# Optimization experiments

Measured on AMD Instinct MI355X. Metric: run time of the kernel, lower is better.

The kernel has to match this reference:

```python
import jax, jax.numpy as jnp
import numpy as np

T, B, NHID = 64, 32, 768
NB, BS = 6, 128          # num_blocks, block_size = nhid // num_blocks
TOPK = 4                 # active blocks per step
NTOK = 32000
ATT = 4 * BS             # input-attention value dim (att_out), per RIMs BlocksCore
DK = 64                  # input-attention key dim
NH2, DK2 = 4, 16         # communication attention heads / head dim


def setup_inputs() -> dict:
    key = jax.random.key(0)
    ks = jax.random.split(key, 16)
    s = 0.02
    return {
        "x": jax.random.normal(ks[0], (T, B, NHID), jnp.float32),
        "hx0": jax.random.normal(ks[1], (B, NHID), jnp.float32),
        "cx0": jax.random.normal(ks[2], (B, NHID), jnp.float32),
        # input attention (1 head): per-read-block query proj, per-write-slot key/value proj
        "Wq_in": jax.random.normal(ks[3], (NB, BS, DK), jnp.float32) * s,
        "Wk_in": jax.random.normal(ks[4], (2, NHID, DK), jnp.float32) * s,
        "Wv_in": jax.random.normal(ks[5], (2, NHID, ATT), jnp.float32) * s,
        # block-diagonal LSTM (blockify_params): per-block weights
        "Wih": jax.random.normal(ks[6], (NB, ATT, 4 * BS), jnp.float32) * s,
        "Whh": jax.random.normal(ks[7], (NB, BS, 4 * BS), jnp.float32) * s,
        "b_lstm": jnp.zeros((NB, 4 * BS), jnp.float32),
        # communication attention (4 heads, dk=dv=16), per-block projections + output proj
        "Wq_c": jax.random.normal(ks[8], (NB, BS, NH2 * DK2), jnp.float32) * s,
        "Wk_c": jax.random.normal(ks[9], (NB, BS, NH2 * DK2), jnp.float32) * s,
        "Wv_c": jax.random.normal(ks[10], (NB, BS, NH2 * DK2), jnp.float32) * s,
        "Wo_c": jax.random.normal(ks[11], (NB, NH2 * DK2, BS), jnp.float32) * s,
        # decoder
        "Wd": jax.random.normal(ks[12], (NTOK, NHID), jnp.float32) * 0.1,
        "bd": jnp.zeros((NTOK,), jnp.float32),
    }


def _step(hx, cx, xt, Wq_in, Wk_in, Wv_in, Wih, Whh, b_lstm, Wq_c, Wk_c, Wv_c, Wo_c):
    hb = hx.reshape(B, NB, BS)
    cb = cx.reshape(B, NB, BS)
    # --- input attention: each block reads from {null, input} slots ---
    kv_in = jnp.stack([jnp.zeros_like(xt), xt], axis=1)          # [B,2,NHID]
    q = jnp.einsum('bnd,ndk->bnk', hb, Wq_in)                    # [B,NB,DK]
    k = jnp.einsum('bmd,mdk->bmk', kv_in, Wk_in)                 # [B,2,DK]
    v = jnp.einsum('bmd,mdv->bmv', kv_in, Wv_in)                 # [B,2,ATT]
    iatt = jax.nn.softmax(
        jnp.einsum('bnk,bmk->bnm', q, k) / jnp.sqrt(jnp.float32(DK)), axis=-1)
    inp_use = jnp.einsum('bnm,bmv->bnv', iatt, v)                # [B,NB,ATT]
    # --- top-k block routing: drop NB-TOPK blocks attending most to null ---
    null_att = iatt[:, :, 0]                                     # [B,NB]
    _, drop_idx = jax.lax.top_k(null_att, NB - TOPK)
    mask = jnp.ones((B, NB), hx.dtype).at[
        jnp.arange(B)[:, None], drop_idx].set(0.0)               # [B,NB]
    # --- per-block (block-diagonal) LSTM ---
    gates = (jnp.einsum('bnv,nvg->bng', inp_use, Wih)
             + jnp.einsum('bnh,nhg->bng', hb, Whh) + b_lstm)     # [B,NB,4*BS]
    i, f, g, o = jnp.split(gates, 4, axis=-1)
    c_new = jax.nn.sigmoid(f) * cb + jax.nn.sigmoid(i) * jnp.tanh(g)
    h_new = jax.nn.sigmoid(o) * jnp.tanh(c_new)                  # [B,NB,BS]
    # --- communication attention among blocks (residual) ---
    q2 = jnp.einsum('bnd,ndk->bnk', h_new, Wq_c).reshape(B, NB, NH2, DK2)
    k2 = jnp.einsum('bnd,ndk->bnk', h_new, Wk_c).reshape(B, NB, NH2, DK2)
    v2 = jnp.einsum('bnd,ndk->bnk', h_new, Wv_c).reshape(B, NB, NH2, DK2)
    att = jax.nn.softmax(
        jnp.einsum('bihk,bjhk->bhij', q2, k2) / jnp.sqrt(jnp.float32(DK2)), axis=-1)
    comm = jnp.einsum('bhij,bjhv->bihv', att, v2).reshape(B, NB, NH2 * DK2)
    h_new = h_new + jnp.einsum('bnk,nkd->bnd', comm, Wo_c)
    # --- gated state update: inactive blocks keep old state ---
    m = mask[:, :, None]
    hx_next = (m * h_new + (1.0 - m) * hb).reshape(B, NHID)
    cx_next = (m * c_new + (1.0 - m) * cb).reshape(B, NHID)
    return hx_next, cx_next


def reference(x, hx0, cx0, Wq_in, Wk_in, Wv_in, Wih, Whh, b_lstm,
              Wq_c, Wk_c, Wv_c, Wo_c, Wd, bd):
    def scan_step(carry, xt):
        hx, cx = carry
        hx, cx = _step(hx, cx, xt, Wq_in, Wk_in, Wv_in, Wih, Whh, b_lstm,
                       Wq_c, Wk_c, Wv_c, Wo_c)
        return (hx, cx), hx
    (hx, cx), outs = jax.lax.scan(scan_step, (hx0, cx0), x)     # outs: [T,B,NHID]
    decoded = outs.reshape(T * B, NHID) @ Wd.T + bd              # [T*B,NTOK]
    return decoded, hx, cx
```

## Files before the change

### kernel.cpp

```cpp
#include <hip/hip_runtime.h>
#include <hip/hip_bf16.h>
#include <stdint.h>

#define TT 64
#define BB 32
#define NHIDC 768
#define NBK 6
#define BSZ 128
#define NTOKC 32000

using f32x4  = __attribute__((ext_vector_type(4))) float;
using f32x2  = __attribute__((ext_vector_type(2))) float;
using short8 = __attribute__((ext_vector_type(8))) short;
typedef unsigned long long u64;

#define OFF_XPUB  4096u
#define OFF_HTB   8065024u
#define OFF_K1    11210752u
#define OFF_V1    11735040u
#define OFF_U     15929344u
#define OFF_WDB   41095168u

__device__ __forceinline__ float sigf(float x){ return 1.f/(1.f + expf(-x)); }

__device__ __forceinline__ void stp(u64* p, float v, unsigned tag){
  union { float f; unsigned u; } cv; cv.f = v;
  const u64 pk = ((u64)tag << 32) | cv.u;
  __hip_atomic_store(p, pk, __ATOMIC_RELAXED, __HIP_MEMORY_SCOPE_AGENT);
}
__device__ __forceinline__ float ldp(const u64* p, unsigned tag){
  u64 v = __hip_atomic_load(p, __ATOMIC_RELAXED, __HIP_MEMORY_SCOPE_AGENT);
  while ((unsigned)(v >> 32) < tag){
    __builtin_amdgcn_s_sleep(1);
    v = __hip_atomic_load(p, __ATOMIC_RELAXED, __HIP_MEMORY_SCOPE_AGENT);
  }
  union { unsigned u; float f; } cv; cv.u = (unsigned)v;
  return cv.f;
}
#define CBAR asm volatile("" ::: "memory")

__device__ __forceinline__ void gload16(const void* g, void* l){
  __builtin_amdgcn_global_load_lds(
      (const __attribute__((address_space(1))) unsigned int*)g,
      (__attribute__((address_space(3))) unsigned int*)l, 16, 0, 0);
}

__device__ __forceinline__ int xslot(int par, int gg, int nn, int b){
  return (((par*16 + gg)*6 + nn)*2 + b)*132;
}

template<int TM, int TN>
__device__ void gemm_tile(const float* __restrict__ A, int lda,
                          const float* __restrict__ Bb, int ldb,
                          float* __restrict__ Cb, int ldc,
                          int N, int K, int m0, int n0,
                          float* AsP, float* BsP, int tid)
{
  constexpr int BM = 16*TM, BN = 16*TN;
  float (*As)[BM]   = reinterpret_cast<float(*)[BM]>(AsP);
  float (*Bs)[BN+4] = reinterpret_cast<float(*)[BN+4]>(BsP);
  const int tx = tid & 15, ty = tid >> 4;
  float acc[TM][TN];
  #pragma unroll
  for (int i=0;i<TM;++i)
    #pragma unroll
    for (int j=0;j<TN;++j) acc[i][j]=0.f;

  for (int k0=0; k0<K; k0+=16){
    if constexpr (TM == 8){
      const int r = tid>>1, kk = (tid&1)*8;
      const float4 v0 = *(const float4*)&A[(long)(m0+r)*lda + k0 + kk];
      const float4 v1 = *(const float4*)&A[(long)(m0+r)*lda + k0 + kk + 4];
      As[kk+0][r]=v0.x; As[kk+1][r]=v0.y; As[kk+2][r]=v0.z; As[kk+3][r]=v0.w;
      As[kk+4][r]=v1.x; As[kk+5][r]=v1.y; As[kk+6][r]=v1.z; As[kk+7][r]=v1.w;
    } else {
      const int r = tid>>2, kk = (tid&3)*4;
      const float4 v0 = *(const float4*)&A[(long)(m0+r)*lda + k0 + kk];
      As[kk+0][r]=v0.x; As[kk+1][r]=v0.y; As[kk+2][r]=v0.z; As[kk+3][r]=v0.w;
    }
    if constexpr (TN == 8){
      const int rb = tid>>4, cb = (tid&15)*8;
      float4 v0 = {0,0,0,0}, v1 = {0,0,0,0};
      if (n0+cb+4 <= N) v0 = *(const float4*)&Bb[(long)(k0+rb)*ldb + n0+cb];
      if (n0+cb+8 <= N) v1 = *(const float4*)&Bb[(long)(k0+rb)*ldb + n0+cb+4];
      *(float4*)&Bs[rb][cb]   = v0;
      *(float4*)&Bs[rb][cb+4] = v1;
    } else {
      const int rb = tid>>4, cb = (tid&15)*4;
      float4 v0 = {0,0,0,0};
      if (n0+cb+4 <= N) v0 = *(const float4*)&Bb[(long)(k0+rb)*ldb + n0+cb];
      *(float4*)&Bs[rb][cb] = v0;
    }
    __syncthreads();
    #pragma unroll
    for (int kk=0; kk<16; ++kk){
      float av[TM], bv[TN];
      #pragma unroll
      for (int i=0;i<TM;++i) av[i] = As[kk][ty*TM+i];
      #pragma unroll
      for (int j=0;j<TN;++j) bv[j] = Bs[kk][tx*TN+j];
      #pragma unroll
      for (int i=0;i<TM;++i)
        #pragma unroll
        for (int j=0;j<TN;++j) acc[i][j] += av[i]*bv[j];
    }
    __syncthreads();
  }
  #pragma unroll
  for (int i=0;i<TM;++i){
    const int row = m0 + ty*TM + i;
    #pragma unroll
    for (int j=0;j<TN;++j){
      const int col = n0 + tx*TN + j;
      if (col < N) Cb[(long)row*ldc + col] = acc[i][j];
    }
  }
}

__global__ __launch_bounds__(256) void pre1_kernel(
    const float* __restrict__ x,
    const float* __restrict__ Wk_in, const float* __restrict__ Wv_in,
    float* __restrict__ K1b, float* __restrict__ V1b,
    u64* __restrict__ xpub)
{
  __shared__ float As[16*128];
  __shared__ float Bs[16*132];
  const int bid = blockIdx.x, tid = threadIdx.x;
  if (bid < 32){
    gemm_tile<4,4>(x, 768, Wk_in + 768*64, 64, K1b, 64, 64, 768,
                   bid*64, 0, As, Bs, tid);
  } else if (bid < 288){
    const int v = bid - 32;
    gemm_tile<4,4>(x, 768, Wv_in + 768*512, 512, V1b, 512, 512, 768,
                   (v>>3)*64, (v&7)*64, As, Bs, tid);
  } else {
    const int nx = 2*16*6*2*132;
    for (int i = (bid-288)*256 + tid; i < nx; i += 64*256)
      __hip_atomic_store(&xpub[i], 0ull, __ATOMIC_RELAXED, __HIP_MEMORY_SCOPE_AGENT);
  }
}

__global__ __launch_bounds__(256) void pre2_kernel(
    const float* __restrict__ V1b, const float* __restrict__ Wih,
    const float* __restrict__ Wd,
    float* __restrict__ Ub, unsigned short* __restrict__ Wdb)
{
  __shared__ float As[16*128];
  __shared__ float Bs[16*132];
  const int bid = blockIdx.x, tid = threadIdx.x;
  if (bid < 384){
    const int m = bid/24, r = bid%24, nt = r/6, z = r%6;
    gemm_tile<8,8>(V1b, 512, Wih + (long)z*262144, 512,
                   Ub + (long)z*512, 3072, 512, 512, m*128, nt*128,
                   As, Bs, tid);
  } else {
    const long n4 = (long)NTOKC*NHIDC/4;
    for (long i = (long)(bid-384)*256 + tid; i < n4; i += (long)512*256){
      const float4 v = ((const float4*)Wd)[i];
      ushort4 o;
      __hip_bfloat16 b0 = __float2bfloat16(v.x); o.x = *reinterpret_cast<unsigned short*>(&b0);
      __hip_bfloat16 b1 = __float2bfloat16(v.y); o.y = *reinterpret_cast<unsigned short*>(&b1);
      __hip_bfloat16 b2 = __float2bfloat16(v.z); o.z = *reinterpret_cast<unsigned short*>(&b2);
      __hip_bfloat16 b3 = __float2bfloat16(v.w); o.w = *reinterpret_cast<unsigned short*>(&b3);
      ((ushort4*)Wdb)[i] = o;
    }
  }
}

__global__ __launch_bounds__(1024, 2) void recurrent_kernel(
    const float* __restrict__ hx0, const float* __restrict__ cx0,
    const float* __restrict__ Wq_in, const float* __restrict__ Whh,
    const float* __restrict__ b_lstm,
    const float* __restrict__ Wk_c, const float* __restrict__ Wv_c,
    const float* __restrict__ Wq_c, const float* __restrict__ Wo_c,
    const float* __restrict__ K1buf, const float* __restrict__ Ubuf,
    u64* __restrict__ xpub,
    unsigned short* __restrict__ HTx,
    float* __restrict__ out_hx, float* __restrict__ out_cx)
{
  const int w = blockIdx.x, gg = w/6, n = w - gg*6, tid = threadIdx.x;

  __shared__ float WcT[192*130];
  __shared__ float WqL[128*65];
  __shared__ float hL[2][128], cL[2][128], h0L[2][128], cnL[2][128];
  __shared__ float partL[2][2][512];
  __shared__ float uL[2][512];
  __shared__ float blL[512];
  __shared__ float kvqL[2][192];
  __shared__ float kvAll[2][6][130];
  __shared__ float commL[2][64];
  __shared__ float nullAll[2][8];
  __shared__ float sL[2], nullLoc[2], maskL[2];

  const int kh = tid >> 9, gc = tid & 511;
  const int od = tid >> 3, okq = tid & 7;

  f32x4 whr[16];
  {
    const float* src = Whh + (long)n*65536 + kh*64*512 + gc;
    #pragma unroll
    for (int r4=0; r4<16; ++r4){
      f32x4 v;
      v[0] = src[(r4*4+0)*512]; v[1] = src[(r4*4+1)*512];
      v[2] = src[(r4*4+2)*512]; v[3] = src[(r4*4+3)*512];
      whr[r4] = v;
    }
  }
  #pragma unroll
  for (int i=0;i<16;++i) asm volatile("" : "+v"(whr[i]));
  f32x4 wo0, wo1;
  {
    const float* src = Wo_c + n*8192 + od;
    #pragma unroll
    for (int j=0;j<4;++j) wo0[j] = src[(okq*8+j)*128];
    #pragma unroll
    for (int j=0;j<4;++j) wo1[j] = src[(okq*8+4+j)*128];
  }
  asm volatile("" : "+v"(wo0));
  asm volatile("" : "+v"(wo1));

  if (tid < 512) blL[tid] = b_lstm[n*512 + tid];
  for (int i = tid; i < 8192; i += 1024){
    const int h = i>>6, c = i&63;
    WcT[(c    )*130 + h] = Wk_c[n*8192 + i];
    WcT[(c+ 64)*130 + h] = Wv_c[n*8192 + i];
    WcT[(c+128)*130 + h] = Wq_c[n*8192 + i];
    WqL[h*65 + c] = Wq_in[n*8192 + i];
  }
  if (tid < 256){
    const int b = tid>>7, d = tid&127;
    hL[b][d] = hx0[(gg*2+b)*768 + n*128 + d];
    cL[b][d] = cx0[(gg*2+b)*768 + n*128 + d];
  }
  __syncthreads();

  for (int t = 0; t < TT; ++t){
    const int par = t & 1;
    const unsigned tag = (unsigned)(t+1);
    uL[kh][gc] = Ubuf[((long)(t*32 + gg*2 + kh)*6 + n)*512 + gc];
    float k1r = 0.f;
    if (tid < 128) k1r = K1buf[(long)(t*32 + gg*2 + (tid>>6))*64 + (tid&63)];

    {
      float gd0 = 0.f, gd1 = 0.f;
      #pragma unroll
      for (int r4 = 0; r4 < 16; ++r4){
        const f32x4 h0v = *(const f32x4*)&hL[0][kh*64 + r4*4];
        const f32x4 h1v = *(const f32x4*)&hL[1][kh*64 + r4*4];
        #pragma unroll
        for (int j=0;j<4;++j){
          gd0 += whr[r4][j]*h0v[j];
          gd1 += whr[r4][j]*h1v[j];
        }
      }
      partL[0][kh][gc] = gd0;
      partL[1][kh][gc] = gd1;
    }
    if (tid < 128){
      const int b = tid>>6, k = tid&63;
      float q = 0.f;
      #pragma unroll 16
      for (int h=0; h<128; ++h) q += WqL[h*65 + k]*hL[b][h];
      float term = q*k1r;
      #pragma unroll
      for (int off=32; off; off>>=1) term += __shfl_xor(term, off);
      if (k == 0){
        const float l1 = term*0.125f;
        const float mx = fmaxf(l1, 0.f);
        const float e0 = expf(0.f-mx), e1 = expf(l1-mx);
        const float inv = 1.f/(e0+e1);
        sL[b] = e1*inv;
        nullLoc[b] = e0*inv;
        stp(xpub + xslot(par,gg,n,b) + 128, e0*inv, tag);
      }
    }
    __syncthreads();
    if (tid < 256){
      const int b = tid>>7, dd = tid&127;
      const float s = sL[b];
      const float gi = partL[b][0][dd]     + partL[b][1][dd]     + s*uL[b][dd]     + blL[dd];
      const float gf = partL[b][0][128+dd] + partL[b][1][128+dd] + s*uL[b][128+dd] + blL[128+dd];
      const float gG = partL[b][0][256+dd] + partL[b][1][256+dd] + s*uL[b][256+dd] + blL[256+dd];
      const float go = partL[b][0][384+dd] + partL[b][1][384+dd] + s*uL[b][384+dd] + blL[384+dd];
      const float cp = cL[b][dd];
      const float cn = sigf(gf)*cp + sigf(gi)*tanhf(gG);
      const float h0 = sigf(go)*tanhf(cn);
      cnL[b][dd] = cn; h0L[b][dd] = h0;
    }
    __syncthreads();
    if (tid < 384){
      const int b = tid/192, c = tid%192;
      float a = 0.f;
      #pragma unroll
      for (int h4=0; h4<32; ++h4){
        const f32x2 wa = *(const f32x2*)&WcT[c*130 + h4*4];
        const f32x2 wb = *(const f32x2*)&WcT[c*130 + h4*4 + 2];
        const f32x4 hv = *(const f32x4*)&h0L[b][h4*4];
        a += wa[0]*hv[0] + wa[1]*hv[1] + wb[0]*hv[2] + wb[1]*hv[3];
      }
      kvqL[b][c] = a;
      if (c < 128) stp(xpub + xslot(par,gg,n,b) + c, a, tag);
    }
    __syncthreads();
    for (int idx = tid; idx < 1536; idx += 1024){
      const int j = idx/256, r = idx&255, b = r>>7, c = r&127;
      if (j == n) kvAll[b][j][c] = kvqL[b][c];
      else        kvAll[b][j][c] = ldp(xpub + xslot(par,gg,j,b) + c, tag);
    }
    if (tid < 12){
      const int j = tid>>1, b = tid&1;
      if (j == n) nullAll[b][j] = nullLoc[b];
      else        nullAll[b][j] = ldp(xpub + xslot(par,gg,j,b) + 128, tag);
    }
    __syncthreads(); CBAR;
    if (tid < 64){
      const int lane = tid;
      const int g5 = lane>>3, l3 = lane&7;
      const int b = g5>>2, h = g5&3;
      float lg = -1e30f;
      if (l3 < 6){
        float s = 0.f;
        #pragma unroll
        for (int kk=0; kk<16; ++kk)
          s += kvqL[b][128 + h*16 + kk]*kvAll[b][l3][h*16 + kk];
        lg = s*0.25f;
      }
      float mx = lg;
      mx = fmaxf(mx, __shfl_xor(mx,1));
      mx = fmaxf(mx, __shfl_xor(mx,2));
      mx = fmaxf(mx, __shfl_xor(mx,4));
      float ev = (l3 < 6) ? expf(lg - mx) : 0.f;
      float sum = ev;
      sum += __shfl_xor(sum,1); sum += __shfl_xor(sum,2); sum += __shfl_xor(sum,4);
      const float myw = ev/sum;
      float s0 = 0.f, s1 = 0.f;
      #pragma unroll
      for (int j=0;j<6;++j){
        const float wj = __shfl(myw, g5*8 + j);
        s0 += wj*kvAll[b][j][64 + h*16 + l3*2];
        s1 += wj*kvAll[b][j][64 + h*16 + l3*2 + 1];
      }
      commL[b][h*16 + l3*2]     = s0;
      commL[b][h*16 + l3*2 + 1] = s1;
      if (lane < 2){
        const float own = nullAll[lane][n];
        int rank = 0;
        #pragma unroll
        for (int j=0;j<6;++j){
          const float v = nullAll[lane][j];
          rank += (v > own || (v == own && j < n)) ? 1 : 0;
        }
        maskL[lane] = (rank < 2) ? 0.f : 1.f;
      }
    }
    __syncthreads();
    {
      #pragma unroll
      for (int b=0; b<2; ++b){
        float a = 0.f;
        #pragma unroll
        for (int j=0;j<4;++j) a += commL[b][okq*8+j]*wo0[j];
        #pragma unroll
        for (int j=0;j<4;++j) a += commL[b][okq*8+4+j]*wo1[j];
        a += __shfl_xor(a,1); a += __shfl_xor(a,2); a += __shfl_xor(a,4);
        if (okq == 0 && maskL[b] != 0.f){
          hL[b][od] = h0L[b][od] + a;
          cL[b][od] = cnL[b][od];
        }
      }
    }
    __syncthreads();
    if (tid < 256){
      const int b = tid>>7, d = tid&127;
      const float hv = hL[b][d];
      __hip_bfloat16 hb16 = __float2bfloat16(hv);
      HTx[(long)(t*32 + gg*2 + b)*768 + n*128 + d] = *reinterpret_cast<unsigned short*>(&hb16);
      if (t == TT-1){
        out_hx[(gg*2+b)*768 + n*128 + d] = hv;
        out_cx[(gg*2+b)*768 + n*128 + d] = cL[b][d];
      }
    }
  }
}

__global__ __launch_bounds__(256) void decoder_kernel(
    const unsigned short* __restrict__ A,
    const unsigned short* __restrict__ Bw,
    const float* __restrict__ bd,
    float* __restrict__ out)
{
  __shared__ unsigned short As[8192];
  __shared__ unsigned short Bs[8192];
  const int bid = blockIdx.x;
  const int tile = (bid & 7)*500 + (bid >> 3);
  const int m0 = (tile & 15)*128, n0 = (tile >> 4)*128;
  const int tid = threadIdx.x;
  const int wv = tid >> 6, lane = tid & 63;
  const int wm = wv >> 1, wn = wv & 1;
  const int r16 = lane & 15, krow = lane >> 4;

  f32x4 acc[4][4] = {};

  for (int k0 = 0; k0 < 768; k0 += 64){
    #pragma unroll
    for (int i=0; i<4; ++i){
      const int idx = i*256 + tid;
      const int row = idx >> 3, cp = idx & 7;
      const int csrc = cp ^ (row & 7);
      gload16(&A [(long)(m0+row)*768 + k0 + csrc*8], (char*)As + i*4096 + wv*1024);
      gload16(&Bw[(long)(n0+row)*768 + k0 + csrc*8], (char*)Bs + i*4096 + wv*1024);
    }
    __syncthreads();
    short8 af[4][2], bf[4][2];
    #pragma unroll
    for (int mi=0; mi<4; ++mi){
      const int row = wm*64 + mi*16 + r16;
      #pragma unroll
      for (int ks=0; ks<2; ++ks){
        const int kc = ks*4 + krow;
        af[mi][ks] = *(const short8*)&As[row*64 + ((kc ^ (row&7))<<3)];
      }
    }
    #pragma unroll
    for (int ni=0; ni<4; ++ni){
      const int row = wn*64 + ni*16 + r16;
      #pragma unroll
      for (int ks=0; ks<2; ++ks){
        const int kc = ks*4 + krow;
        bf[ni][ks] = *(const short8*)&Bs[row*64 + ((kc ^ (row&7))<<3)];
      }
    }
    #pragma unroll
    for (int mi=0; mi<4; ++mi)
      #pragma unroll
      for (int ni=0; ni<4; ++ni){
        acc[mi][ni] = __builtin_amdgcn_mfma_f32_16x16x32_bf16(af[mi][0], bf[ni][0], acc[mi][ni], 0, 0, 0);
        acc[mi][ni] = __builtin_amdgcn_mfma_f32_16x16x32_bf16(af[mi][1], bf[ni][1], acc[mi][ni], 0, 0, 0);
      }
    __syncthreads();
  }

  #pragma unroll
  for (int ni=0; ni<4; ++ni){
    const int col = n0 + wn*64 + ni*16 + r16;
    const float bv = bd[col];
    #pragma unroll
    for (int mi=0; mi<4; ++mi){
      const int rbase = m0 + wm*64 + mi*16 + krow*4;
      #pragma unroll
      for (int j=0; j<4; ++j)
        out[(size_t)(rbase + j)*NTOKC + col] = acc[mi][ni][j] + bv;
    }
  }
}

extern "C" void kernel_launch(void* const* d_in, const int* in_sizes, int n_in,
                              void* d_out, int out_size, void* d_ws, size_t ws_size,
                              hipStream_t stream)
{
  (void)in_sizes; (void)n_in; (void)out_size; (void)ws_size;
  const float* x      = (const float*)d_in[0];
  const float* hx0    = (const float*)d_in[1];
  const float* cx0    = (const float*)d_in[2];
  const float* Wq_in  = (const float*)d_in[3];
  const float* Wk_in  = (const float*)d_in[4];
  const float* Wv_in  = (const float*)d_in[5];
  const float* Wih    = (const float*)d_in[6];
  const float* Whh    = (const float*)d_in[7];
  const float* b_lstm = (const float*)d_in[8];
  const float* Wq_c   = (const float*)d_in[9];
  const float* Wk_c   = (const float*)d_in[10];
  const float* Wv_c   = (const float*)d_in[11];
  const float* Wo_c   = (const float*)d_in[12];
  const float* Wd     = (const float*)d_in[13];
  const float* bd     = (const float*)d_in[14];

  char* ws = (char*)d_ws;
  u64*           xpub = (u64*)(ws + OFF_XPUB);
  unsigned short* HTx = (unsigned short*)(ws + OFF_HTB);
  float*         K1b  = (float*)(ws + OFF_K1);
  float*         V1b  = (float*)(ws + OFF_V1);
  float*         Ub   = (float*)(ws + OFF_U);
  unsigned short* Wdb = (unsigned short*)(ws + OFF_WDB);

  float* out_dec = (float*)d_out;
  float* out_hx  = out_dec + (size_t)2048*NTOKC;
  float* out_cx  = out_hx + BB*NHIDC;

  pre1_kernel<<<352, 256, 0, stream>>>(x, Wk_in, Wv_in, K1b, V1b, xpub);
  pre2_kernel<<<896, 256, 0, stream>>>(V1b, Wih, Wd, Ub, Wdb);
  recurrent_kernel<<<96, 1024, 0, stream>>>(hx0, cx0, Wq_in, Whh, b_lstm,
                                            Wk_c, Wv_c, Wq_c, Wo_c,
                                            K1b, Ub, xpub, HTx,
                                            out_hx, out_cx);
  decoder_kernel<<<4000, 256, 0, stream>>>(HTx, Wdb, bd, out_dec);
}
```

Baseline: 1.219 ms.

## Compute U projection with split-bf16 MFMA instead of fp32 FMA GEMM

```diff
diff --git a/kernel.cpp b/kernel.cpp
--- a/kernel.cpp
+++ b/kernel.cpp
@@ -15,9 +15,12 @@
 typedef unsigned long long u64;
 
 #define OFF_XPUB  4096u
+#define OFF_WTH   1048576u
+#define OFF_WTL   4194304u
 #define OFF_HTB   8065024u
 #define OFF_K1    11210752u
-#define OFF_V1    11735040u
+#define OFF_V1H   11735040u
+#define OFF_V1L   13832192u
 #define OFF_U     15929344u
 #define OFF_WDB   41095168u
 
@@ -47,6 +50,14 @@
 
 __device__ __forceinline__ int xslot(int par, int gg, int nn, int b){
   return (((par*16 + gg)*6 + nn)*2 + b)*132;
+}
+
+__device__ __forceinline__ void split_hl(float v, unsigned short& h16, unsigned short& l16){
+  __hip_bfloat16 h = __float2bfloat16(v);
+  float hv = __bfloat162float(h);
+  __hip_bfloat16 l = __float2bfloat16(v - hv);
+  h16 = *reinterpret_cast<unsigned short*>(&h);
+  l16 = *reinterpret_cast<unsigned short*>(&l);
 }
 
 template<int TM, int TN>
@@ -67,25 +78,12 @@
     for (int j=0;j<TN;++j) acc[i][j]=0.f;
 
   for (int k0=0; k0<K; k0+=16){
-    if constexpr (TM == 8){
-      const int r = tid>>1, kk = (tid&1)*8;
-      const float4 v0 = *(const float4*)&A[(long)(m0+r)*lda + k0 + kk];
-      const float4 v1 = *(const float4*)&A[(long)(m0+r)*lda + k0 + kk + 4];
-      As[kk+0][r]=v0.x; As[kk+1][r]=v0.y; As[kk+2][r]=v0.z; As[kk+3][r]=v0.w;
-      As[kk+4][r]=v1.x; As[kk+5][r]=v1.y; As[kk+6][r]=v1.z; As[kk+7][r]=v1.w;
-    } else {
+    {
       const int r = tid>>2, kk = (tid&3)*4;
       const float4 v0 = *(const float4*)&A[(long)(m0+r)*lda + k0 + kk];
       As[kk+0][r]=v0.x; As[kk+1][r]=v0.y; As[kk+2][r]=v0.z; As[kk+3][r]=v0.w;
     }
-    if constexpr (TN == 8){
-      const int rb = tid>>4, cb = (tid&15)*8;
-      float4 v0 = {0,0,0,0}, v1 = {0,0,0,0};
-      if (n0+cb+4 <= N) v0 = *(const float4*)&Bb[(long)(k0+rb)*ldb + n0+cb];
-      if (n0+cb+8 <= N) v1 = *(const float4*)&Bb[(long)(k0+rb)*ldb + n0+cb+4];
-      *(float4*)&Bs[rb][cb]   = v0;
-      *(float4*)&Bs[rb][cb+4] = v1;
-    } else {
+    {
       const int rb = tid>>4, cb = (tid&15)*4;
       float4 v0 = {0,0,0,0};
       if (n0+cb+4 <= N) v0 = *(const float4*)&Bb[(long)(k0+rb)*ldb + n0+cb];
@@ -117,45 +115,173 @@
   }
 }
 
+__device__ void gemm_tile_v1(const float* __restrict__ A,
+                             const float* __restrict__ Bb,
+                             unsigned short* __restrict__ V1H,
+                             unsigned short* __restrict__ V1L,
+                             int m0, int n0,
+                             float* AsP, float* BsP, int tid)
+{
+  float (*As)[64] = reinterpret_cast<float(*)[64]>(AsP);
+  float (*Bs)[68] = reinterpret_cast<float(*)[68]>(BsP);
+  const int tx = tid & 15, ty = tid >> 4;
+  float acc[4][4];
+  #pragma unroll
+  for (int i=0;i<4;++i)
+    #pragma unroll
+    for (int j=0;j<4;++j) acc[i][j]=0.f;
+
+  for (int k0=0; k0<768; k0+=16){
+    {
+      const int r = tid>>2, kk = (tid&3)*4;
+      const float4 v0 = *(const float4*)&A[(long)(m0+r)*768 + k0 + kk];
+      As[kk+0][r]=v0.x; As[kk+1][r]=v0.y; As[kk+2][r]=v0.z; As[kk+3][r]=v0.w;
+    }
+    {
+      const int rb = tid>>4, cb = (tid&15)*4;
+      const float4 v0 = *(const float4*)&Bb[(long)(k0+rb)*512 + n0+cb];
+      *(float4*)&Bs[rb][cb] = v0;
+    }
+    __syncthreads();
+    #pragma unroll
+    for (int kk=0; kk<16; ++kk){
+      float av[4], bv[4];
+      #pragma unroll
+      for (int i=0;i<4;++i) av[i] = As[kk][ty*4+i];
+      #pragma unroll
+      for (int j=0;j<4;++j) bv[j] = Bs[kk][tx*4+j];
+      #pragma unroll
+      for (int i=0;i<4;++i)
+        #pragma unroll
+        for (int j=0;j<4;++j) acc[i][j] += av[i]*bv[j];
+    }
+    __syncthreads();
+  }
+  #pragma unroll
+  for (int i=0;i<4;++i){
+    const int row = m0 + ty*4 + i;
+    const int col0 = n0 + tx*4;
+    ushort4 oh, ol;
+    split_hl(acc[i][0], oh.x, ol.x);
+    split_hl(acc[i][1], oh.y, ol.y);
+    split_hl(acc[i][2], oh.z, ol.z);
+    split_hl(acc[i][3], oh.w, ol.w);
+    *(ushort4*)&V1H[(long)row*512 + col0] = oh;
+    *(ushort4*)&V1L[(long)row*512 + col0] = ol;
+  }
+}
+
 __global__ __launch_bounds__(256) void pre1_kernel(
     const float* __restrict__ x,
     const float* __restrict__ Wk_in, const float* __restrict__ Wv_in,
-    float* __restrict__ K1b, float* __restrict__ V1b,
+    const float* __restrict__ Wih,
+    float* __restrict__ K1b,
+    unsigned short* __restrict__ V1H, unsigned short* __restrict__ V1L,
+    unsigned short* __restrict__ WTH, unsigned short* __restrict__ WTL,
     u64* __restrict__ xpub)
 {
-  __shared__ float As[16*128];
-  __shared__ float Bs[16*132];
+  __shared__ float As[16*64];
+  __shared__ float Bs[16*68];
+  __shared__ float T[64][65];
   const int bid = blockIdx.x, tid = threadIdx.x;
   if (bid < 32){
     gemm_tile<4,4>(x, 768, Wk_in + 768*64, 64, K1b, 64, 64, 768,
                    bid*64, 0, As, Bs, tid);
   } else if (bid < 288){
     const int v = bid - 32;
-    gemm_tile<4,4>(x, 768, Wv_in + 768*512, 512, V1b, 512, 512, 768,
-                   (v>>3)*64, (v&7)*64, As, Bs, tid);
-  } else {
+    gemm_tile_v1(x, Wv_in + 768*512, V1H, V1L,
+                 (v>>3)*64, (v&7)*64, As, Bs, tid);
+  } else if (bid < 352){
     const int nx = 2*16*6*2*132;
     for (int i = (bid-288)*256 + tid; i < nx; i += 64*256)
       __hip_atomic_store(&xpub[i], 0ull, __ATOMIC_RELAXED, __HIP_MEMORY_SCOPE_AGENT);
+  } else {
+    const int tb = bid - 352;
+    const int z = tb>>6, tile = tb&63, kt = (tile>>3)<<6, ct = (tile&7)<<6;
+    const float* src = Wih + (long)z*262144;
+    #pragma unroll 4
+    for (int i=0;i<16;++i){
+      const int idx = i*256+tid, rr = idx>>6, cc = idx&63;
+      T[rr][cc] = src[(long)(kt+rr)*512 + ct+cc];
+    }
+    __syncthreads();
+    #pragma unroll 4
+    for (int i=0;i<16;++i){
+      const int idx = i*256+tid, cr = idx>>6, kk = idx&63;
+      unsigned short h16, l16;
+      split_hl(T[kk][cr], h16, l16);
+      WTH[(long)z*262144 + (long)(ct+cr)*512 + kt+kk] = h16;
+      WTL[(long)z*262144 + (long)(ct+cr)*512 + kt+kk] = l16;
+    }
   }
 }
 
 __global__ __launch_bounds__(256) void pre2_kernel(
-    const float* __restrict__ V1b, const float* __restrict__ Wih,
+    const unsigned short* __restrict__ V1H, const unsigned short* __restrict__ V1L,
+    const unsigned short* __restrict__ WTH, const unsigned short* __restrict__ WTL,
     const float* __restrict__ Wd,
     float* __restrict__ Ub, unsigned short* __restrict__ Wdb)
 {
-  __shared__ float As[16*128];
-  __shared__ float Bs[16*132];
+  __shared__ unsigned short AH[4096], AL[4096], BH[4096], BL[4096];
   const int bid = blockIdx.x, tid = threadIdx.x;
   if (bid < 384){
-    const int m = bid/24, r = bid%24, nt = r/6, z = r%6;
-    gemm_tile<8,8>(V1b, 512, Wih + (long)z*262144, 512,
-                   Ub + (long)z*512, 3072, 512, 512, m*128, nt*128,
-                   As, Bs, tid);
+    const int z = bid%6, mt = (bid/6)%16, nt2 = bid/96;
+    const int m0 = mt*128, n0 = nt2*128;
+    const int wv = tid>>6, lane = tid&63;
+    const int wm = wv>>1, wn = wv&1;
+    const int r16 = lane&15, krow = lane>>4;
+    f32x4 acc[4][4] = {};
+    const unsigned short* Bh = WTH + (long)z*262144;
+    const unsigned short* Bl = WTL + (long)z*262144;
+
+    for (int k0 = 0; k0 < 512; k0 += 32){
+      #pragma unroll
+      for (int i=0; i<2; ++i){
+        const int idx = i*256 + tid;
+        const int row = idx >> 2, k8 = (idx & 3)*8;
+        gload16(&V1H[(long)(m0+row)*512 + k0 + k8], (char*)AH + i*4096 + wv*1024);
+        gload16(&V1L[(long)(m0+row)*512 + k0 + k8], (char*)AL + i*4096 + wv*1024);
+        gload16(&Bh [(long)(n0+row)*512 + k0 + k8], (char*)BH + i*4096 + wv*1024);
+        gload16(&Bl [(long)(n0+row)*512 + k0 + k8], (char*)BL + i*4096 + wv*1024);
+      }
+      __syncthreads();
+      short8 ah[4], al[4], bh[4], bl[4];
+      #pragma unroll
+      for (int mi=0; mi<4; ++mi){
+        const int off = (wm*64 + mi*16 + r16)*32 + krow*8;
+        ah[mi] = *(const short8*)&AH[off];
+        al[mi] = *(const short8*)&AL[off];
+      }
+      #pragma unroll
+      for (int ni=0; ni<4; ++ni){
+        const int off = (wn*64 + ni*16 + r16)*32 + krow*8;
+        bh[ni] = *(const short8*)&BH[off];
+        bl[ni] = *(const short8*)&BL[off];
+      }
+      #pragma unroll
+      for (int mi=0; mi<4; ++mi)
+        #pragma unroll
+        for (int ni=0; ni<4; ++ni){
+          acc[mi][ni] = __builtin_amdgcn_mfma_f32_16x16x32_bf16(ah[mi], bh[ni], acc[mi][ni], 0, 0, 0);
+          acc[mi][ni] = __builtin_amdgcn_mfma_f32_16x16x32_bf16(ah[mi], bl[ni], acc[mi][ni], 0, 0, 0);
+          acc[mi][ni] = __builtin_amdgcn_mfma_f32_16x16x32_bf16(al[mi], bh[ni], acc[mi][ni], 0, 0, 0);
+        }
+      __syncthreads();
+    }
+    #pragma unroll
+    for (int ni=0; ni<4; ++ni){
+      const int col = n0 + wn*64 + ni*16 + r16;
+      #pragma unroll
+      for (int mi=0; mi<4; ++mi){
+        const int rbase = m0 + wm*64 + mi*16 + krow*4;
+        #pragma unroll
+        for (int j=0; j<4; ++j)
+          Ub[(long)(rbase + j)*3072 + z*512 + col] = acc[mi][ni][j];
+      }
+    }
   } else {
     const long n4 = (long)NTOKC*NHIDC/4;
-    for (long i = (long)(bid-384)*256 + tid; i < n4; i += (long)512*256){
+    for (long i = (long)(bid-384)*256 + tid; i < n4; i += (long)384*256){
       const float4 v = ((const float4*)Wd)[i];
       ushort4 o;
       __hip_bfloat16 b0 = __float2bfloat16(v.x); o.x = *reinterpret_cast<unsigned short*>(&b0);
@@ -477,9 +603,12 @@
 
   char* ws = (char*)d_ws;
   u64*           xpub = (u64*)(ws + OFF_XPUB);
+  unsigned short* WTH = (unsigned short*)(ws + OFF_WTH);
+  unsigned short* WTL = (unsigned short*)(ws + OFF_WTL);
   unsigned short* HTx = (unsigned short*)(ws + OFF_HTB);
   float*         K1b  = (float*)(ws + OFF_K1);
-  float*         V1b  = (float*)(ws + OFF_V1);
+  unsigned short* V1H = (unsigned short*)(ws + OFF_V1H);
+  unsigned short* V1L = (unsigned short*)(ws + OFF_V1L);
   float*         Ub   = (float*)(ws + OFF_U);
   unsigned short* Wdb = (unsigned short*)(ws + OFF_WDB);
 
@@ -487,8 +616,9 @@
   float* out_hx  = out_dec + (size_t)2048*NTOKC;
   float* out_cx  = out_hx + BB*NHIDC;
 
-  pre1_kernel<<<352, 256, 0, stream>>>(x, Wk_in, Wv_in, K1b, V1b, xpub);
-  pre2_kernel<<<896, 256, 0, stream>>>(V1b, Wih, Wd, Ub, Wdb);
+  pre1_kernel<<<736, 256, 0, stream>>>(x, Wk_in, Wv_in, Wih, K1b,
+                                       V1H, V1L, WTH, WTL, xpub);
+  pre2_kernel<<<768, 256, 0, stream>>>(V1H, V1L, WTH, WTL, Wd, Ub, Wdb);
   recurrent_kernel<<<96, 1024, 0, stream>>>(hx0, cx0, Wq_in, Whh, b_lstm,
                                             Wk_c, Wv_c, Wq_c, Wo_c,
                                             K1b, Ub, xpub, HTx,
```

New measurement: 1.127 ms, median of 2. 1.08x faster.
